# Kernel tuning notes

Measured on AMD Instinct MI355X. Metric: run time of the kernel, lower is better.

## Reference

```python
import jax, jax.numpy as jnp
import numpy as np

N = 8192
H = 256
E = N * 32
ALPHA = 0.2  # LeakyReLU negative slope from init kwarg alpha


def setup_inputs() -> dict:
    key = jax.random.key(0)
    ks = jax.random.split(key, 8)
    s = 1.0 / np.sqrt(H)
    return {
        "features": jax.random.normal(ks[0], (N, H), jnp.float32),
        "edge_index": jax.random.randint(ks[1], (2, E), 0, N, jnp.int64),
        "W_att": jax.random.normal(ks[2], (H, H), jnp.float32) * s,
        "a_src": jax.random.normal(ks[3], (H,), jnp.float32) * s,
        "a_dst": jax.random.normal(ks[4], (H,), jnp.float32) * s,
        "gcn_w": jax.random.normal(ks[5], (H, H), jnp.float32) * s,
        "gcn_b": jnp.zeros((H,), jnp.float32),
        "out_w": jax.random.normal(ks[6], (H, 2), jnp.float32) * s,
        "out_b": jnp.zeros((2,), jnp.float32),
    }


def reference(features, edge_index, W_att, a_src, a_dst, gcn_w, gcn_b, out_w, out_b):
    n = features.shape[0]
    # --- SingleNodeAttentionLayer (GAT-style dense self-attention, concat=True) ---
    Wh = features @ W_att                       # [N, H]
    e = jax.nn.leaky_relu(
        (Wh @ a_src)[:, None] + (Wh @ a_dst)[None, :], negative_slope=ALPHA
    )                                            # [N, N]
    attn = jax.nn.softmax(e, axis=-1)
    h1 = jax.nn.elu(attn @ Wh)                   # [N, H]
    # --- GCNConv: symmetric-normalized aggregation with self-loops ---
    loops = jnp.arange(n, dtype=edge_index.dtype)
    row = jnp.concatenate([edge_index[0], loops])  # destination
    col = jnp.concatenate([edge_index[1], loops])  # source
    deg = jax.ops.segment_sum(jnp.ones_like(row, dtype=h1.dtype), row, num_segments=n)
    dinv = jax.lax.rsqrt(jnp.maximum(deg, 1e-12))
    norm = dinv[row] * dinv[col]                 # [E+N]
    x = h1 @ gcn_w                               # [N, H]
    agg = jax.ops.segment_sum(x[col] * norm[:, None], row, num_segments=n) + gcn_b
    # --- head: linear -> mean over nodes -> softmax ---
    res = agg @ out_w + out_b                    # [N, 2]
    res = jnp.mean(res, axis=0, keepdims=True)   # [1, 2]
    return jax.nn.softmax(res, axis=-1)
```

## Files before the change

kernel.cpp:

```cpp
#include <hip/hip_runtime.h>
#include <hip/hip_bf16.h>

#define NN 8192
#define HH 256
#define EE (NN*32)
#define ALPHAC 0.2f
#define CHUNK 16
#define NCHUNK (NN/CHUNK)
#define CSPAD 1024

typedef __bf16 bf16x8 __attribute__((ext_vector_type(8)));
typedef float  f32x4  __attribute__((ext_vector_type(4)));

#define OFF_WH     0
#define OFF_S      (OFF_WH + NN*HH)
#define OFF_D      (OFF_S + NN)
#define OFF_SORTD  (OFF_D + NN)
#define OFF_PERM   (OFF_SORTD + NN)
#define OFF_EA     (OFF_PERM + NN)
#define OFF_E1     (OFF_EA + NN)
#define OFF_SAREL  (OFF_E1 + NN)
#define OFF_SBREL  (OFF_SAREL + NN)
#define OFF_ABPART (OFF_SBREL + NN)
#define OFF_CPAB   (OFF_ABPART + 2*NN*HH)
#define OFF_CSA    (OFF_CPAB + 2*(NCHUNK+1)*HH)
#define OFF_CSB    (OFF_CSA + CSPAD)
#define OFF_DEG    (OFF_CSB + CSPAD)
#define OFF_V      (OFF_DEG + NN)
#define OFF_DINV   (OFF_V + HH)
#define OFF_WNODE  (OFF_DINV + NN)
#define OFF_KEYS   (OFF_WNODE + NN)
#define OFF_FB16   (OFF_KEYS + 2*NN)
#define OFF_WT16   (OFF_FB16 + NN*HH/2)
#define OFF_CNT    (OFF_WT16 + HH*HH/2)
#define OFF_KI     (OFF_CNT + 16)
#define OFF_WAS    (OFF_KI + NN)
#define OFF_WAD    (OFF_WAS + HH)

__device__ __forceinline__ float elu1(float x) {
    return x > 0.f ? x : (expf(x) - 1.f);
}

__device__ __forceinline__ unsigned long long thresh_key(float t) {
    unsigned u = __float_as_uint(t);
    unsigned mono = u ^ ((u & 0x80000000u) ? 0xFFFFFFFFu : 0x80000000u);
    return ((unsigned long long)mono + 1ULL) << 13;
}

__global__ __launch_bounds__(256) void k_prep(const float* __restrict__ features,
                                              const float* __restrict__ W_att,
                                              const float* __restrict__ a_src,
                                              const float* __restrict__ a_dst,
                                              float* ws) {
    int bid = blockIdx.x, tid = threadIdx.x;
    int wave = tid >> 6, lane = tid & 63;
    if (bid < 1024) {
        int base = (bid*256 + tid)*8;
        float4 a = *(const float4*)(features + base);
        float4 b = *(const float4*)(features + base + 4);
        bf16x8 v;
        v[0]=(__bf16)a.x; v[1]=(__bf16)a.y; v[2]=(__bf16)a.z; v[3]=(__bf16)a.w;
        v[4]=(__bf16)b.x; v[5]=(__bf16)b.y; v[6]=(__bf16)b.z; v[7]=(__bf16)b.w;
        *(bf16x8*)((__bf16*)(ws + OFF_FB16) + base) = v;
    } else if (bid < 1056) {
        int idx0 = ((bid-1024)*256 + tid)*8;
        __bf16* WT = (__bf16*)(ws + OFF_WT16);
        #pragma unroll
        for (int q = 0; q < 8; ++q) {
            int idx = idx0 + q;
            int n = idx >> 8, k = idx & 255;
            WT[idx] = (__bf16)W_att[(size_t)k*HH + n];
        }
    } else if (bid < 1120) {
        int k = (bid - 1056)*4 + wave;
        float4 w = *(const float4*)(W_att + (size_t)k*HH + lane*4);
        float4 as = *(const float4*)(a_src + lane*4);
        float4 ad = *(const float4*)(a_dst + lane*4);
        float ss = w.x*as.x + w.y*as.y + w.z*as.z + w.w*as.w;
        float dd = w.x*ad.x + w.y*ad.y + w.z*ad.z + w.w*ad.w;
        #pragma unroll
        for (int off = 32; off; off >>= 1) {
            ss += __shfl_xor(ss, off);
            dd += __shfl_xor(dd, off);
        }
        if (lane == 0) {
            ws[OFF_WAS + k] = ss;
            ws[OFF_WAD + k] = dd;
        }
    } else {
        int z0 = ((bid-1120)*256 + tid);
        if (z0 < NN + HH) ws[OFF_DEG + z0] = 0.f;
        if (bid == 1120 && tid < 16) ((unsigned*)(ws + OFF_CNT))[tid] = 0u;
    }
}

__global__ __launch_bounds__(256) void k_gemm_deg_sd(const float* __restrict__ features,
                                                     const int* __restrict__ ei, float* ws) {
    int bid = blockIdx.x, tid = threadIdx.x;
    int wave = tid >> 6, lane = tid & 63;
    if (bid < 512) {
        int mt = bid >> 2, nt = bid & 3;
        int ml = lane & 15, quad = lane >> 4;
        int row0 = mt*64 + wave*16;
        int n0 = nt*64;
        const __bf16* FB = (const __bf16*)(ws + OFF_FB16);
        const __bf16* WT = (const __bf16*)(ws + OFF_WT16);
        const __bf16* Ap = FB + (size_t)(row0 + ml)*HH + quad*8;
        const __bf16* B0 = WT + (size_t)(n0 +  0 + ml)*HH + quad*8;
        const __bf16* B1 = WT + (size_t)(n0 + 16 + ml)*HH + quad*8;
        const __bf16* B2 = WT + (size_t)(n0 + 32 + ml)*HH + quad*8;
        const __bf16* B3 = WT + (size_t)(n0 + 48 + ml)*HH + quad*8;
        f32x4 ac0 = {0.f,0.f,0.f,0.f}, ac1 = ac0, ac2 = ac0, ac3 = ac0;
        #pragma unroll
        for (int k0 = 0; k0 < HH; k0 += 32) {
            bf16x8 af = *(const bf16x8*)(Ap + k0);
            ac0 = __builtin_amdgcn_mfma_f32_16x16x32_bf16(af, *(const bf16x8*)(B0 + k0), ac0, 0, 0, 0);
            ac1 = __builtin_amdgcn_mfma_f32_16x16x32_bf16(af, *(const bf16x8*)(B1 + k0), ac1, 0, 0, 0);
            ac2 = __builtin_amdgcn_mfma_f32_16x16x32_bf16(af, *(const bf16x8*)(B2 + k0), ac2, 0, 0, 0);
            ac3 = __builtin_amdgcn_mfma_f32_16x16x32_bf16(af, *(const bf16x8*)(B3 + k0), ac3, 0, 0, 0);
        }
        float* Whp = ws + OFF_WH;
        #pragma unroll
        for (int r = 0; r < 4; ++r) {
            size_t grow = (size_t)(row0 + quad*4 + r)*HH + n0 + ml;
            Whp[grow +  0] = ac0[r];
            Whp[grow + 16] = ac1[r];
            Whp[grow + 32] = ac2[r];
            Whp[grow + 48] = ac3[r];
        }
    } else {
        int b = bid - 512;
        int e = b*512 + tid;
        atomicAdd(ws + OFF_DEG + ei[e], 1.0f);
        atomicAdd(ws + OFF_DEG + ei[e + 256], 1.0f);
        float4 as = *(const float4*)(ws + OFF_WAS + lane*4);
        float4 ad = *(const float4*)(ws + OFF_WAD + lane*4);
        int row0 = b*16 + wave*4;
        #pragma unroll
        for (int r = 0; r < 4; ++r) {
            int row = row0 + r;
            float4 f = *(const float4*)(features + (size_t)row*HH + lane*4);
            float ss = f.x*as.x + f.y*as.y + f.z*as.z + f.w*as.w;
            float dd = f.x*ad.x + f.y*ad.y + f.z*ad.z + f.w*ad.w;
            #pragma unroll
            for (int off = 32; off; off >>= 1) {
                ss += __shfl_xor(ss, off);
                dd += __shfl_xor(dd, off);
            }
            if (lane == 0) {
                ws[OFF_S+row] = ss; ws[OFF_D+row] = dd;
                unsigned u = __float_as_uint(dd);
                unsigned mono = u ^ ((u & 0x80000000u) ? 0xFFFFFFFFu : 0x80000000u);
                ((unsigned long long*)(ws + OFF_KEYS))[row] =
                    (((unsigned long long)mono) << 13) | (unsigned)row;
            }
        }
    }
}

__global__ __launch_bounds__(256) void k_rank_dinv(float* ws) {
    __shared__ unsigned long long lk[NN];
    int bid = blockIdx.x, tid = threadIdx.x;
    int wave = tid >> 6, lane = tid & 63;
    if (bid < 512) {
        const unsigned long long* keys = (const unsigned long long*)(ws + OFF_KEYS);
        for (int m = tid; m < NN/2; m += 256)
            *(ulonglong2*)&lk[m*2] = *(const ulonglong2*)&keys[m*2];
        __syncthreads();
        int jb = bid*16 + wave*4;
        unsigned long long kj0 = lk[jb+0], kj1 = lk[jb+1];
        unsigned long long kj2 = lk[jb+2], kj3 = lk[jb+3];
        unsigned long long tk0 = thresh_key(-ws[OFF_S + jb+0]);
        unsigned long long tk1 = thresh_key(-ws[OFF_S + jb+1]);
        unsigned long long tk2 = thresh_key(-ws[OFF_S + jb+2]);
        unsigned long long tk3 = thresh_key(-ws[OFF_S + jb+3]);
        int c0 = 0, c1 = 0, c2 = 0, c3 = 0;
        int t0 = 0, t1 = 0, t2 = 0, t3 = 0;
        #pragma unroll 4
        for (int it = 0; it < 64; ++it) {
            ulonglong2 kq = *(const ulonglong2*)&lk[(it*64 + lane)*2];
            c0 += (kq.x < kj0); c1 += (kq.x < kj1);
            c2 += (kq.x < kj2); c3 += (kq.x < kj3);
            t0 += (kq.x < tk0); t1 += (kq.x < tk1);
            t2 += (kq.x < tk2); t3 += (kq.x < tk3);
            c0 += (kq.y < kj0); c1 += (kq.y < kj1);
            c2 += (kq.y < kj2); c3 += (kq.y < kj3);
            t0 += (kq.y < tk0); t1 += (kq.y < tk1);
            t2 += (kq.y < tk2); t3 += (kq.y < tk3);
        }
        #pragma unroll
        for (int off = 1; off < 64; off <<= 1) {
            c0 += __shfl_xor(c0, off);
            c1 += __shfl_xor(c1, off);
            c2 += __shfl_xor(c2, off);
            c3 += __shfl_xor(c3, off);
            t0 += __shfl_xor(t0, off);
            t1 += __shfl_xor(t1, off);
            t2 += __shfl_xor(t2, off);
            t3 += __shfl_xor(t3, off);
        }
        if (lane == 0) {
            unsigned long long kk[4] = {kj0, kj1, kj2, kj3};
            int cr[4] = {c0, c1, c2, c3};
            int tr[4] = {t0, t1, t2, t3};
            #pragma unroll
            for (int q = 0; q < 4; ++q) {
                unsigned long long kv = kk[q];
                int r = cr[q];
                unsigned mm = (unsigned)(kv >> 13);
                unsigned u = (mm & 0x80000000u) ? (mm ^ 0x80000000u) : ~mm;
                float dj = __uint_as_float(u);
                int j = (int)(kv & 8191ULL);
                ws[OFF_SORTD + r] = dj;
                ((int*)ws)[OFF_PERM + r] = j;
                ws[OFF_EA + r] = expf(ALPHAC * dj);
                ws[OFF_E1 + r] = expf(dj);
                ((int*)ws)[OFF_KI + jb + q] = tr[q];
            }
        }
    } else {
        int i = (bid - 512)*256 + tid;
        float dv = rsqrtf(ws[OFF_DEG + i] + 1.0f);
        ws[OFF_DINV + i] = dv;
        ws[OFF_WNODE + i] = dv*dv;
    }
}

__global__ __launch_bounds__(256) void k_wnode_vecpref(const int* __restrict__ ei, float* ws) {
    int bid = blockIdx.x, tid = threadIdx.x;
    if (bid < NCHUNK) {
        __shared__ int   sp[CHUNK];
        __shared__ float sea[CHUNK], se1[CHUNK];
        int c = bid, h = tid;
        int k0 = c * CHUNK;
        if (h < CHUNK) {
            sp[h]  = ((int*)ws)[OFF_PERM + k0 + h];
            sea[h] = ws[OFF_EA + k0 + h];
            se1[h] = ws[OFF_E1 + k0 + h];
        }
        __syncthreads();
        if (tid < 64) {
            int lane = tid;
            float v = 0.f;
            if (lane < 16) v = sea[lane];
            else if (lane < 32) v = se1[lane-16];
            #pragma unroll
            for (int off = 1; off < 16; off <<= 1) {
                float x = __shfl_up(v, off);
                if ((lane & 15) >= off) v += x;
            }
            if (lane < 16) {
                ws[OFF_SAREL + k0 + lane] = v;
                if (lane == 15) ws[OFF_CSA + c + 1] = v;
            } else if (lane < 32) {
                ws[OFF_SBREL + k0 + lane - 16] = v;
                if (lane == 31) ws[OFF_CSB + c + 1] = v;
            }
        }
        const float* Wh = ws + OFF_WH;
        float wv[CHUNK];
        #pragma unroll
        for (int kk = 0; kk < CHUNK; ++kk)
            wv[kk] = Wh[(size_t)sp[kk]*HH + h];
        float2* abp = (float2*)(ws + OFF_ABPART);
        float acca = 0.f, accb = 0.f;
        #pragma unroll
        for (int kk = 0; kk < CHUNK; ++kk) {
            acca += sea[kk]*wv[kk]; accb += se1[kk]*wv[kk];
            abp[(size_t)(k0+kk)*HH + h] = make_float2(acca, accb);
        }
        float2* cp = (float2*)(ws + OFF_CPAB);
        cp[(size_t)(c+1)*HH + h] = make_float2(acca, accb);
    } else {
        int e = (bid - NCHUNK)*512 + tid;
        int r0 = ei[e],       c0i = ei[EE + e];
        int r1 = ei[e + 256], c1i = ei[EE + e + 256];
        atomicAdd(ws + OFF_WNODE + c0i, ws[OFF_DINV + r0] * ws[OFF_DINV + c0i]);
        atomicAdd(ws + OFF_WNODE + c1i, ws[OFF_DINV + r1] * ws[OFF_DINV + c1i]);
    }
}

__global__ __launch_bounds__(256) void k_chunkscan(float* ws) {
    int bid = blockIdx.x, tid = threadIdx.x;
    if (bid < 32) {
        int h = bid*8 + (tid >> 5);
        int t = tid & 31;
        float2* cp = (float2*)(ws + OFF_CPAB);
        float la[16], lb[16];
        float ta = 0.f, tb = 0.f;
        #pragma unroll
        for (int m = 0; m < 16; ++m) {
            float2 v = cp[(size_t)(t*16 + m + 1)*HH + h];
            la[m] = v.x; lb[m] = v.y;
            ta += la[m]; tb += lb[m];
        }
        float ia = ta, ib = tb;
        #pragma unroll
        for (int off = 1; off < 32; off <<= 1) {
            float xa = __shfl_up(ia, off, 32);
            float xb = __shfl_up(ib, off, 32);
            if (t >= off) { ia += xa; ib += xb; }
        }
        float ba = ia - ta, bb = ib - tb;
        #pragma unroll
        for (int m = 0; m < 16; ++m) {
            cp[(size_t)(t*16 + m)*HH + h] = make_float2(ba, bb);
            ba += la[m]; bb += lb[m];
        }
        if (t == 31) cp[(size_t)NCHUNK*HH + h] = make_float2(ba, bb);
    } else {
        int lane = tid & 63, wvi = tid >> 6;
        bool act = wvi < 2;
        float* cs = ws + (wvi == 1 ? OFF_CSB : OFF_CSA);
        float la[8];
        float ta = 0.f;
        if (act) {
            #pragma unroll
            for (int m = 0; m < 8; ++m) { la[m] = cs[lane*8 + m + 1]; ta += la[m]; }
        }
        float ia = ta;
        #pragma unroll
        for (int off = 1; off < 64; off <<= 1) {
            float x = __shfl_up(ia, off);
            if (lane >= off) ia += x;
        }
        float ba = ia - ta;
        __syncthreads();
        if (act) {
            #pragma unroll
            for (int m = 0; m < 8; ++m) { cs[lane*8 + m] = ba; ba += la[m]; }
            if (lane == 63) cs[NCHUNK] = ba;
        }
    }
}

__global__ __launch_bounds__(256) void k_rows_final(
        const float* __restrict__ gcn_w, const float* __restrict__ gcn_b,
        const float* __restrict__ out_w, const float* __restrict__ out_b,
        float* ws, float* out) {
    __shared__ float red[4][256];
    __shared__ float fin[3*256];
    __shared__ int islast;
    int tid = threadIdx.x;
    int wave = tid >> 6, lane = tid & 63;
    int gw = blockIdx.x*4 + wave;
    const float2* abp  = (const float2*)(ws + OFF_ABPART);
    const float2* cpab = (const float2*)(ws + OFF_CPAB);
    float btot = ws[OFF_CSB + NCHUNK];
    const float4* btr = (const float4*)(cpab + (size_t)NCHUNK*HH);
    float4 bt0 = btr[lane*2], bt1 = btr[lane*2+1];
    float BTx = bt0.y, BTy = bt0.w, BTz = bt1.y, BTw = bt1.w;

    float accx = 0.f, accy = 0.f, accz = 0.f, accw = 0.f;
    #pragma unroll
    for (int r = 0; r < 4; ++r) {
        int i = gw*4 + r;
        int k = ((const int*)ws)[OFF_KI + i];
        float si = ws[OFF_S + i];
        float eas = expf(ALPHAC * si), es = expf(si);
        float av = 0.f, bv = 0.f;
        float Ax=0.f, Ay=0.f, Az=0.f, Aw=0.f, Bx=0.f, By=0.f, Bz=0.f, Bw=0.f;
        if (k > 0) {
            int km = k - 1, cc = km >> 4;
            av = ws[OFF_CSA + cc] + ws[OFF_SAREL + km];
            bv = ws[OFF_CSB + cc] + ws[OFF_SBREL + km];
            const float4* pr = (const float4*)(abp + (size_t)km*HH);
            const float4* cr = (const float4*)(cpab + (size_t)cc*HH);
            float4 p0 = pr[lane*2], p1 = pr[lane*2+1];
            float4 q0 = cr[lane*2], q1 = cr[lane*2+1];
            Ax = p0.x + q0.x; Bx = p0.y + q0.y;
            Ay = p0.z + q0.z; By = p0.w + q0.w;
            Az = p1.x + q1.x; Bz = p1.y + q1.y;
            Aw = p1.z + q1.z; Bw = p1.w + q1.w;
        }
        float Z = eas*av + es*(btot - bv);
        float invZ = 1.f / Z;
        float w = ws[OFF_WNODE + i];
        accx += w * elu1((eas*Ax + es*(BTx - Bx)) * invZ);
        accy += w * elu1((eas*Ay + es*(BTy - By)) * invZ);
        accz += w * elu1((eas*Az + es*(BTz - Bz)) * invZ);
        accw += w * elu1((eas*Aw + es*(BTw - Bw)) * invZ);
    }
    red[wave][lane*4+0] = accx;
    red[wave][lane*4+1] = accy;
    red[wave][lane*4+2] = accz;
    red[wave][lane*4+3] = accw;
    __syncthreads();
    float sum = red[0][tid] + red[1][tid] + red[2][tid] + red[3][tid];
    atomicAdd(ws + OFF_V + tid, sum);

    __syncthreads();
    if (tid == 0) {
        unsigned* cnt = (unsigned*)(ws + OFF_CNT);
        unsigned arrived = __hip_atomic_fetch_add(&cnt[0], 1u,
                               __ATOMIC_ACQ_REL, __HIP_MEMORY_SCOPE_AGENT) + 1u;
        islast = (arrived == (unsigned)(NN/16));
    }
    __syncthreads();
    if (islast) {
        float* vl  = fin;
        float* r0s = fin + 256;
        float* r1s = fin + 512;
        int t = tid;
        vl[t] = __hip_atomic_load(ws + OFF_V + t, __ATOMIC_RELAXED,
                                  __HIP_MEMORY_SCOPE_AGENT);
        __syncthreads();
        float acc = 0.f;
        for (int h = 0; h < HH; ++h) acc += vl[h] * gcn_w[(size_t)h*HH + t];
        float meanv = acc * (1.0f/(float)NN) + gcn_b[t];
        r0s[t] = meanv * out_w[t*2+0];
        r1s[t] = meanv * out_w[t*2+1];
        __syncthreads();
        for (int off = 128; off; off >>= 1) {
            if (t < off) { r0s[t] += r0s[t+off]; r1s[t] += r1s[t+off]; }
            __syncthreads();
        }
        if (t == 0) {
            float res0 = r0s[0] + out_b[0], res1 = r1s[0] + out_b[1];
            float m = fmaxf(res0, res1);
            float e0 = expf(res0 - m), e1v = expf(res1 - m);
            float inv = 1.f / (e0 + e1v);
            out[0] = e0 * inv;
            out[1] = e1v * inv;
        }
    }
}

extern "C" void kernel_launch(void* const* d_in, const int* in_sizes, int n_in,
                              void* d_out, int out_size, void* d_ws, size_t ws_size,
                              hipStream_t stream) {
    const float* features = (const float*)d_in[0];
    const int*   eidx     = (const int*)d_in[1];
    const float* W_att    = (const float*)d_in[2];
    const float* a_src    = (const float*)d_in[3];
    const float* a_dst    = (const float*)d_in[4];
    const float* gcn_w    = (const float*)d_in[5];
    const float* gcn_b    = (const float*)d_in[6];
    const float* out_w    = (const float*)d_in[7];
    const float* out_b    = (const float*)d_in[8];
    float* ws  = (float*)d_ws;
    float* out = (float*)d_out;

    k_prep<<<1154, 256, 0, stream>>>(features, W_att, a_src, a_dst, ws);
    k_gemm_deg_sd<<<1024, 256, 0, stream>>>(features, eidx, ws);
    k_rank_dinv<<<544, 256, 0, stream>>>(ws);
    k_wnode_vecpref<<<1024, 256, 0, stream>>>(eidx, ws);
    k_chunkscan<<<33, 256, 0, stream>>>(ws);
    k_rows_final<<<NN/16, 256, 0, stream>>>(gcn_w, gcn_b, out_w, out_b, ws, out);
}
```

Before: 165.3 us.

## Privatize atomic accumulators into slices and double final-kernel block count

```diff
diff --git a/kernel.cpp b/kernel.cpp
--- a/kernel.cpp
+++ b/kernel.cpp
@@ -36,6 +36,10 @@
 #define OFF_KI     (OFF_CNT + 16)
 #define OFF_WAS    (OFF_KI + NN)
 #define OFF_WAD    (OFF_WAS + HH)
+#define OFF_DEG8   (OFF_WAD + HH)
+#define OFF_WN8    (OFF_DEG8 + 8*NN)
+#define OFF_V16    (OFF_WN8 + 8*NN)
+#define ZERO_FLOATS (8*NN + 16*HH)
 
 __device__ __forceinline__ float elu1(float x) {
     return x > 0.f ? x : (expf(x) - 1.f);
@@ -88,8 +92,11 @@
             ws[OFF_WAD + k] = dd;
         }
     } else {
-        int z0 = ((bid-1120)*256 + tid);
-        if (z0 < NN + HH) ws[OFF_DEG + z0] = 0.f;
+        int q = ((bid-1120)*256 + tid);
+        if (q*4 < ZERO_FLOATS) {
+            float4 z = {0.f,0.f,0.f,0.f};
+            *(float4*)(ws + OFF_DEG8 + q*4) = z;
+        }
         if (bid == 1120 && tid < 16) ((unsigned*)(ws + OFF_CNT))[tid] = 0u;
     }
 }
@@ -131,8 +138,9 @@
     } else {
         int b = bid - 512;
         int e = b*512 + tid;
-        atomicAdd(ws + OFF_DEG + ei[e], 1.0f);
-        atomicAdd(ws + OFF_DEG + ei[e + 256], 1.0f);
+        float* deg = ws + OFF_DEG8 + (size_t)(bid & 7)*NN;
+        atomicAdd(deg + ei[e], 1.0f);
+        atomicAdd(deg + ei[e + 256], 1.0f);
         float4 as = *(const float4*)(ws + OFF_WAS + lane*4);
         float4 ad = *(const float4*)(ws + OFF_WAD + lane*4);
         int row0 = b*16 + wave*4;
@@ -220,9 +228,14 @@
         }
     } else {
         int i = (bid - 512)*256 + tid;
-        float dv = rsqrtf(ws[OFF_DEG + i] + 1.0f);
+        float deg = 0.f;
+        #pragma unroll
+        for (int s = 0; s < 8; ++s) deg += ws[OFF_DEG8 + s*NN + i];
+        float dv = rsqrtf(deg + 1.0f);
         ws[OFF_DINV + i] = dv;
-        ws[OFF_WNODE + i] = dv*dv;
+        ws[OFF_WN8 + i] = dv*dv;
+        #pragma unroll
+        for (int s = 1; s < 8; ++s) ws[OFF_WN8 + s*NN + i] = 0.f;
     }
 }
 
@@ -273,10 +286,11 @@
         cp[(size_t)(c+1)*HH + h] = make_float2(acca, accb);
     } else {
         int e = (bid - NCHUNK)*512 + tid;
+        float* wn = ws + OFF_WN8 + (size_t)(bid & 7)*NN;
         int r0 = ei[e],       c0i = ei[EE + e];
         int r1 = ei[e + 256], c1i = ei[EE + e + 256];
-        atomicAdd(ws + OFF_WNODE + c0i, ws[OFF_DINV + r0] * ws[OFF_DINV + c0i]);
-        atomicAdd(ws + OFF_WNODE + c1i, ws[OFF_DINV + r1] * ws[OFF_DINV + c1i]);
+        atomicAdd(wn + c0i, ws[OFF_DINV + r0] * ws[OFF_DINV + c0i]);
+        atomicAdd(wn + c1i, ws[OFF_DINV + r1] * ws[OFF_DINV + c1i]);
     }
 }
 
@@ -353,8 +367,8 @@
 
     float accx = 0.f, accy = 0.f, accz = 0.f, accw = 0.f;
     #pragma unroll
-    for (int r = 0; r < 4; ++r) {
-        int i = gw*4 + r;
+    for (int r = 0; r < 2; ++r) {
+        int i = gw*2 + r;
         int k = ((const int*)ws)[OFF_KI + i];
         float si = ws[OFF_S + i];
         float eas = expf(ALPHAC * si), es = expf(si);
@@ -375,7 +389,9 @@
         }
         float Z = eas*av + es*(btot - bv);
         float invZ = 1.f / Z;
-        float w = ws[OFF_WNODE + i];
+        float w = 0.f;
+        #pragma unroll
+        for (int s = 0; s < 8; ++s) w += ws[OFF_WN8 + s*NN + i];
         accx += w * elu1((eas*Ax + es*(BTx - Bx)) * invZ);
         accy += w * elu1((eas*Ay + es*(BTy - By)) * invZ);
         accz += w * elu1((eas*Az + es*(BTz - Bz)) * invZ);
@@ -387,14 +403,14 @@
     red[wave][lane*4+3] = accw;
     __syncthreads();
     float sum = red[0][tid] + red[1][tid] + red[2][tid] + red[3][tid];
-    atomicAdd(ws + OFF_V + tid, sum);
+    atomicAdd(ws + OFF_V16 + (size_t)(blockIdx.x & 15)*HH + tid, sum);
 
     __syncthreads();
     if (tid == 0) {
         unsigned* cnt = (unsigned*)(ws + OFF_CNT);
         unsigned arrived = __hip_atomic_fetch_add(&cnt[0], 1u,
                                __ATOMIC_ACQ_REL, __HIP_MEMORY_SCOPE_AGENT) + 1u;
-        islast = (arrived == (unsigned)(NN/16));
+        islast = (arrived == 1024u);
     }
     __syncthreads();
     if (islast) {
@@ -402,8 +418,12 @@
         float* r0s = fin + 256;
         float* r1s = fin + 512;
         int t = tid;
-        vl[t] = __hip_atomic_load(ws + OFF_V + t, __ATOMIC_RELAXED,
-                                  __HIP_MEMORY_SCOPE_AGENT);
+        float vv = 0.f;
+        #pragma unroll
+        for (int s = 0; s < 16; ++s)
+            vv += __hip_atomic_load(ws + OFF_V16 + s*HH + t, __ATOMIC_RELAXED,
+                                    __HIP_MEMORY_SCOPE_AGENT);
+        vl[t] = vv;
         __syncthreads();
         float acc = 0.f;
         for (int h = 0; h < HH; ++h) acc += vl[h] * gcn_w[(size_t)h*HH + t];
@@ -441,10 +461,10 @@
     float* ws  = (float*)d_ws;
     float* out = (float*)d_out;
 
-    k_prep<<<1154, 256, 0, stream>>>(features, W_att, a_src, a_dst, ws);
+    k_prep<<<1188, 256, 0, stream>>>(features, W_att, a_src, a_dst, ws);
     k_gemm_deg_sd<<<1024, 256, 0, stream>>>(features, eidx, ws);
     k_rank_dinv<<<544, 256, 0, stream>>>(ws);
     k_wnode_vecpref<<<1024, 256, 0, stream>>>(eidx, ws);
     k_chunkscan<<<33, 256, 0, stream>>>(ws);
-    k_rows_final<<<NN/16, 256, 0, stream>>>(gcn_w, gcn_b, out_w, out_b, ws, out);
-}
+    k_rows_final<<<1024, 256, 0, stream>>>(gcn_w, gcn_b, out_w, out_b, ws, out);
+}
```

After: 170.7 us. 3.3% more time.
